# Kernel optimization log

Hardware: AMD Instinct MI355X
Metric: run time of the kernel (lower is better)

The kernel has to match this reference:

```python
import jax, jax.numpy as jnp
import numpy as np

B, C, H, W = 4, 64, 64, 64
C8 = C // 8
TEMPERATURE = 1.0


def setup_inputs() -> dict:
    key = jax.random.key(0)
    ks = jax.random.split(key, 8)
    x = jax.random.normal(ks[0], (B, C, H, W), jnp.float32)
    s = 1.0 / np.sqrt(C).astype(np.float32)
    wq = jax.random.normal(ks[1], (C8, C), jnp.float32) * s
    bq = jax.random.normal(ks[2], (C8,), jnp.float32) * 0.01
    wk = jax.random.normal(ks[3], (C8, C), jnp.float32) * s
    bk = jax.random.normal(ks[4], (C8,), jnp.float32) * 0.01
    wv = jax.random.normal(ks[5], (C, C), jnp.float32) * s
    bv = jax.random.normal(ks[6], (C,), jnp.float32) * 0.01
    fractal_weight = jnp.asarray(0.5, jnp.float32)
    noise = jax.random.normal(ks[7], (B, H * W, H * W), jnp.float32)
    return {"x": x, "wq": wq, "bq": bq, "wk": wk, "bk": bk,
            "wv": wv, "bv": bv, "fractal_weight": fractal_weight, "noise": noise}


def _conv1x1(x, w, b):
    # 1x1 conv == per-pixel matmul: [B,C,H,W] x [O,C] -> [B,O,H,W]
    return jnp.einsum('bchw,oc->bohw', x, w) + b[None, :, None, None]


def _fractal_reg(amap):
    # amap: [B,1,H,W]; unbiased variance of avg-pooled maps at scales 1,2,4,8
    b, _, h, w = amap.shape
    variances = []
    for s in (1, 2, 4, 8):
        p = amap.reshape(b, 1, h // s, s, w // s, s).mean(axis=(3, 5))  # avg_pool2d
        m = p.mean(axis=(2, 3), keepdims=True)
        n = (h // s) * (w // s)
        variances.append(((p - m) ** 2).sum(axis=(2, 3)) / (n - 1))  # [B,1]
    top = jnp.stack(variances[:-1])
    bot = jnp.stack(variances[1:])
    return (top / bot).mean()


def reference(x, wq, bq, wk, bk, wv, bv, fractal_weight, noise):
    b, c, h, w = x.shape
    n = h * w
    q = _conv1x1(x, wq, bq).reshape(b, -1, n).transpose(0, 2, 1)  # [B,N,C8]
    k = _conv1x1(x, wk, bk).reshape(b, -1, n)                     # [B,C8,N]
    v = _conv1x1(x, wv, bv).reshape(b, -1, n)                     # [B,C,N]
    attn = jax.nn.softmax(jnp.einsum('bnc,bcm->bnm', q, k) * TEMPERATURE, axis=-1)
    chaos = noise * 0.1 * fractal_weight
    attn = jax.nn.softmax(attn + chaos, axis=-1)                  # [B,N,N]
    # out[b,c,i] = sum_j v[b,c,j] * attn[i,j]  (bmm(value, attn^T))
    out = jnp.einsum('bcj,bij->bci', v, attn).reshape(b, c, h, w)
    amap = attn.mean(axis=-1).reshape(b, 1, h, w)
    reg = _fractal_reg(amap)
    return out, reg
```

## Files before the change

kernel.cpp:

```cpp
#include <hip/hip_runtime.h>
#include <hip/hip_bf16.h>
#include <math.h>

#define LOG2E 1.4426950408889634f

typedef __attribute__((ext_vector_type(8))) short short8_t;
typedef __attribute__((ext_vector_type(4))) float float4_t;

union Frag { short8_t f; unsigned u[4]; };

__device__ inline unsigned pack_bf16(float lo, float hi){
  union { __hip_bfloat162 h2; unsigned u; } cv;
  cv.h2 = __float22bfloat162_rn(make_float2(lo, hi));
  return cv.u;
}

__global__ __launch_bounds__(256) void k1_qkv(
    const float* __restrict__ x, const float* __restrict__ wq, const float* __restrict__ bq,
    const float* __restrict__ wk, const float* __restrict__ bk,
    const float* __restrict__ wv, const float* __restrict__ bv,
    float* __restrict__ qs, float* __restrict__ kk, unsigned short* __restrict__ vT,
    float* __restrict__ regout)
{
  int tid = blockIdx.x*256 + threadIdx.x;
  if (tid == 0) regout[0] = 0.f;
  int g = tid >> 14;
  int p = tid & 16383;
  int b = p >> 12, n = p & 4095;
  const float* xp = x + (size_t)b*64*4096 + n;
  float xr[64];
  #pragma unroll
  for (int c=0;c<64;++c) xr[c] = xp[(size_t)c*4096];

  if (g == 0){
    float* qp = qs + ((size_t)b*4096 + n)*8;
    #pragma unroll
    for (int u=0;u<8;++u){
      const float* wr = wq + u*64;
      float a0=0,a1=0,a2=0,a3=0;
      #pragma unroll
      for (int c=0;c<64;c+=4){ a0=fmaf(wr[c],xr[c],a0); a1=fmaf(wr[c+1],xr[c+1],a1);
                               a2=fmaf(wr[c+2],xr[c+2],a2); a3=fmaf(wr[c+3],xr[c+3],a3); }
      qp[u] = (bq[u] + ((a0+a1)+(a2+a3))) * LOG2E;
    }
    #pragma unroll
    for (int u=0;u<8;++u){
      const float* wr = wk + u*64;
      float a0=0,a1=0,a2=0,a3=0;
      #pragma unroll
      for (int c=0;c<64;c+=4){ a0=fmaf(wr[c],xr[c],a0); a1=fmaf(wr[c+1],xr[c+1],a1);
                               a2=fmaf(wr[c+2],xr[c+2],a2); a3=fmaf(wr[c+3],xr[c+3],a3); }
      kk[((size_t)b*8+u)*4096 + n] = bk[u] + ((a0+a1)+(a2+a3));
    }
  } else {
    int c0 = (g==1) ? 0 : (g==2) ? 22 : 43;
    int c1 = (g==1) ? 22 : (g==2) ? 43 : 64;
    for (int u=c0; u<c1; ++u){
      const float* wr = wv + u*64;
      float a0=0,a1=0,a2=0,a3=0;
      #pragma unroll
      for (int c=0;c<64;c+=4){ a0=fmaf(wr[c],xr[c],a0); a1=fmaf(wr[c+1],xr[c+1],a1);
                               a2=fmaf(wr[c+2],xr[c+2],a2); a3=fmaf(wr[c+3],xr[c+3],a3); }
      float res = bv[u] + ((a0+a1)+(a2+a3));
      __hip_bfloat16 h = __float2bfloat16(res);
      vT[((size_t)b*64+u)*4096 + n] = *(unsigned short*)&h;
    }
  }
}

__global__ __launch_bounds__(512, 8) void k3_fused(
    const float* __restrict__ qs, const float* __restrict__ kk,
    const unsigned short* __restrict__ vT, const float* __restrict__ noise,
    const float* __restrict__ fwp, float* __restrict__ out)
{
  __shared__ float lds_l[8][16];
  __shared__ float lds_acc[8][16][64];
  int bid = blockIdx.x;
  int b = bid >> 8; int i0 = (bid & 255) * 16;
  int t = threadIdx.x; int w = t >> 6; int lane = t & 63;
  int li = lane & 15, q4 = lane >> 4;
  int row = i0 + li;
  int jbase = w * 512;

  const float* qp = qs + ((size_t)b*4096 + row)*8;
  float qv[8];
  #pragma unroll
  for (int c=0;c<8;++c) qv[c] = qp[c];
  const float* kkb = kk + (size_t)b*8*4096;
  const float* nzr = noise + ((size_t)b*4096 + row)*4096;
  const unsigned short* vTb = vT + (size_t)b*64*4096;

  float l1 = 0.f;
  for (int sc=0; sc<16; ++sc){
    int j0 = jbase + sc*32 + q4*8;
    float s0=0,s1=0,s2=0,s3=0,s4=0,s5=0,s6=0,s7=0;
    #pragma unroll
    for (int c=0;c<8;++c){
      const float4* kp = (const float4*)(kkb + (size_t)c*4096 + j0);
      float4 ka = kp[0], kb2 = kp[1];
      float q = qv[c];
      s0=fmaf(q,ka.x,s0); s1=fmaf(q,ka.y,s1); s2=fmaf(q,ka.z,s2); s3=fmaf(q,ka.w,s3);
      s4=fmaf(q,kb2.x,s4); s5=fmaf(q,kb2.y,s5); s6=fmaf(q,kb2.z,s6); s7=fmaf(q,kb2.w,s7);
    }
    l1 += exp2f(s0-25.f); l1 += exp2f(s1-25.f); l1 += exp2f(s2-25.f); l1 += exp2f(s3-25.f);
    l1 += exp2f(s4-25.f); l1 += exp2f(s5-25.f); l1 += exp2f(s6-25.f); l1 += exp2f(s7-25.f);
  }
  l1 += __shfl_xor(l1, 16); l1 += __shfl_xor(l1, 32);
  if (lane < 16) lds_l[w][li] = l1;
  __syncthreads();
  float l1tot = 0.f;
  #pragma unroll
  for (int ww=0; ww<8; ++ww) l1tot += lds_l[ww][li];
  float c1 = LOG2E / l1tot;
  float ncoef = 0.1f * fwp[0] * LOG2E;

  float4_t acc0 = {0.f,0.f,0.f,0.f}, acc1 = acc0, acc2 = acc0, acc3 = acc0;
  float l2 = 0.f;
  for (int sc=0; sc<16; ++sc){
    int j0 = jbase + sc*32 + q4*8;
    float s0=0,s1=0,s2=0,s3=0,s4=0,s5=0,s6=0,s7=0;
    #pragma unroll
    for (int c=0;c<8;++c){
      const float4* kp = (const float4*)(kkb + (size_t)c*4096 + j0);
      float4 ka = kp[0], kb2 = kp[1];
      float q = qv[c];
      s0=fmaf(q,ka.x,s0); s1=fmaf(q,ka.y,s1); s2=fmaf(q,ka.z,s2); s3=fmaf(q,ka.w,s3);
      s4=fmaf(q,kb2.x,s4); s5=fmaf(q,kb2.y,s5); s6=fmaf(q,kb2.z,s6); s7=fmaf(q,kb2.w,s7);
    }
    const float4* np = (const float4*)(nzr + j0);
    float4 n0 = np[0], n1 = np[1];
    float p0,p1,p2,p3,p4,p5,p6,p7;
    p0 = exp2f(fmaf(ncoef,n0.x, fmaf(exp2f(s0-25.f), c1, -2.f)));
    p1 = exp2f(fmaf(ncoef,n0.y, fmaf(exp2f(s1-25.f), c1, -2.f)));
    p2 = exp2f(fmaf(ncoef,n0.z, fmaf(exp2f(s2-25.f), c1, -2.f)));
    p3 = exp2f(fmaf(ncoef,n0.w, fmaf(exp2f(s3-25.f), c1, -2.f)));
    p4 = exp2f(fmaf(ncoef,n1.x, fmaf(exp2f(s4-25.f), c1, -2.f)));
    p5 = exp2f(fmaf(ncoef,n1.y, fmaf(exp2f(s5-25.f), c1, -2.f)));
    p6 = exp2f(fmaf(ncoef,n1.z, fmaf(exp2f(s6-25.f), c1, -2.f)));
    p7 = exp2f(fmaf(ncoef,n1.w, fmaf(exp2f(s7-25.f), c1, -2.f)));
    l2 += ((p0+p1)+(p2+p3)) + ((p4+p5)+(p6+p7));
    Frag af;
    af.u[0] = pack_bf16(p0,p1); af.u[1] = pack_bf16(p2,p3);
    af.u[2] = pack_bf16(p4,p5); af.u[3] = pack_bf16(p6,p7);
    const unsigned short* vp = vTb + (size_t)li*4096 + j0;
    short8_t b0 = *(const short8_t*)(vp);
    short8_t b1 = *(const short8_t*)(vp + 16*4096);
    short8_t b2 = *(const short8_t*)(vp + 32*4096);
    short8_t b3 = *(const short8_t*)(vp + 48*4096);
    acc0 = __builtin_amdgcn_mfma_f32_16x16x32_bf16(af.f, b0, acc0, 0, 0, 0);
    acc1 = __builtin_amdgcn_mfma_f32_16x16x32_bf16(af.f, b1, acc1, 0, 0, 0);
    acc2 = __builtin_amdgcn_mfma_f32_16x16x32_bf16(af.f, b2, acc2, 0, 0, 0);
    acc3 = __builtin_amdgcn_mfma_f32_16x16x32_bf16(af.f, b3, acc3, 0, 0, 0);
  }
  l2 += __shfl_xor(l2, 16); l2 += __shfl_xor(l2, 32);
  __syncthreads();
  if (lane < 16) lds_l[w][li] = l2;
  #pragma unroll
  for (int reg=0; reg<4; ++reg){
    int rr = q4*4 + reg;
    lds_acc[w][rr][ 0 + li] = acc0[reg];
    lds_acc[w][rr][16 + li] = acc1[reg];
    lds_acc[w][rr][32 + li] = acc2[reg];
    lds_acc[w][rr][48 + li] = acc3[reg];
  }
  __syncthreads();
  if (t < 256){
    int c = t >> 2, rg = t & 3;
    float4 o;
    float* op = (float*)&o;
    #pragma unroll
    for (int r=0;r<4;++r){
      int rr = rg*4 + r;
      float vsum = 0.f, l2t = 0.f;
      #pragma unroll
      for (int ww=0; ww<8; ++ww){ vsum += lds_acc[ww][rr][c]; l2t += lds_l[ww][rr]; }
      op[r] = vsum / l2t;
    }
    *(float4*)(out + ((size_t)b*64 + c)*4096 + i0 + rg*4) = o;
  }
}

extern "C" void kernel_launch(void* const* d_in, const int* in_sizes, int n_in,
                              void* d_out, int out_size, void* d_ws, size_t ws_size,
                              hipStream_t stream) {
  const float* x     = (const float*)d_in[0];
  const float* wq    = (const float*)d_in[1];
  const float* bq    = (const float*)d_in[2];
  const float* wk    = (const float*)d_in[3];
  const float* bk    = (const float*)d_in[4];
  const float* wv    = (const float*)d_in[5];
  const float* bv    = (const float*)d_in[6];
  const float* fw    = (const float*)d_in[7];
  const float* noise = (const float*)d_in[8];
  float* out = (float*)d_out;
  float* ws  = (float*)d_ws;
  float* qs = ws;
  float* kk = ws + 131072;
  unsigned short* vT = (unsigned short*)(ws + 262144);

  hipLaunchKernelGGL(k1_qkv,   dim3(256),  dim3(256), 0, stream,
                     x,wq,bq,wk,bk,wv,bv,qs,kk,vT, out + 1048576);
  hipLaunchKernelGGL(k3_fused, dim3(1024), dim3(512), 0, stream,
                     qs,kk,vT,noise,fw,out);
}
```

Baseline: 547.6 us.

## Spread QKV projection over more blocks and schedule loads ahead in attention loop

The projection kernel now runs 16 thread groups instead of 4 (q and k each split in two, v split twelve ways), so it launches 1024 blocks for more parallelism, at the cost of re-reading x per group. In the fused attention kernel, the noise and V loads are moved ahead of the score and exp math, and sched_group_barrier hints group VMEM loads and VALU and MFMA work to hide memory latency. Launch bounds drop from 8 to 4 waves per EU, which allows more registers but may reduce occupancy.

New measurement: 540.8 us. About the same (-1.2%).

```diff
diff --git a/kernel.cpp b/kernel.cpp
--- a/kernel.cpp
+++ b/kernel.cpp
@@ -32,10 +32,12 @@
   #pragma unroll
   for (int c=0;c<64;++c) xr[c] = xp[(size_t)c*4096];
 
-  if (g == 0){
+  if (g < 2){
     float* qp = qs + ((size_t)b*4096 + n)*8;
+    int u0 = g*4;
     #pragma unroll
-    for (int u=0;u<8;++u){
+    for (int uu=0;uu<4;++uu){
+      int u = u0 + uu;
       const float* wr = wq + u*64;
       float a0=0,a1=0,a2=0,a3=0;
       #pragma unroll
@@ -43,8 +45,11 @@
                                a2=fmaf(wr[c+2],xr[c+2],a2); a3=fmaf(wr[c+3],xr[c+3],a3); }
       qp[u] = (bq[u] + ((a0+a1)+(a2+a3))) * LOG2E;
     }
+  } else if (g < 4){
+    int u0 = (g-2)*4;
     #pragma unroll
-    for (int u=0;u<8;++u){
+    for (int uu=0;uu<4;++uu){
+      int u = u0 + uu;
       const float* wr = wk + u*64;
       float a0=0,a1=0,a2=0,a3=0;
       #pragma unroll
@@ -53,9 +58,9 @@
       kk[((size_t)b*8+u)*4096 + n] = bk[u] + ((a0+a1)+(a2+a3));
     }
   } else {
-    int c0 = (g==1) ? 0 : (g==2) ? 22 : 43;
-    int c1 = (g==1) ? 22 : (g==2) ? 43 : 64;
-    for (int u=c0; u<c1; ++u){
+    int c0 = ((g-4)*64)/12;
+    int c1v = ((g-3)*64)/12;
+    for (int u=c0; u<c1v; ++u){
       const float* wr = wv + u*64;
       float a0=0,a1=0,a2=0,a3=0;
       #pragma unroll
@@ -68,7 +73,19 @@
   }
 }
 
-__global__ __launch_bounds__(512, 8) void k3_fused(
+
+#define PB_DOT(J0) \
+    float s0=0,s1=0,s2=0,s3=0,s4=0,s5=0,s6=0,s7=0; \
+    _Pragma("unroll") \
+    for (int c=0;c<8;++c){ \
+      const float4* kp = (const float4*)(kkb + (size_t)c*4096 + (J0)); \
+      float4 ka = kp[0], kb2 = kp[1]; \
+      float q = qv[c]; \
+      s0=fmaf(q,ka.x,s0); s1=fmaf(q,ka.y,s1); s2=fmaf(q,ka.z,s2); s3=fmaf(q,ka.w,s3); \
+      s4=fmaf(q,kb2.x,s4); s5=fmaf(q,kb2.y,s5); s6=fmaf(q,kb2.z,s6); s7=fmaf(q,kb2.w,s7); \
+    }
+
+__global__ __launch_bounds__(512, 4) void k3_fused(
     const float* __restrict__ qs, const float* __restrict__ kk,
     const unsigned short* __restrict__ vT, const float* __restrict__ noise,
     const float* __restrict__ fwp, float* __restrict__ out)
@@ -93,17 +110,11 @@
   float l1 = 0.f;
   for (int sc=0; sc<16; ++sc){
     int j0 = jbase + sc*32 + q4*8;
-    float s0=0,s1=0,s2=0,s3=0,s4=0,s5=0,s6=0,s7=0;
-    #pragma unroll
-    for (int c=0;c<8;++c){
-      const float4* kp = (const float4*)(kkb + (size_t)c*4096 + j0);
-      float4 ka = kp[0], kb2 = kp[1];
-      float q = qv[c];
-      s0=fmaf(q,ka.x,s0); s1=fmaf(q,ka.y,s1); s2=fmaf(q,ka.z,s2); s3=fmaf(q,ka.w,s3);
-      s4=fmaf(q,kb2.x,s4); s5=fmaf(q,kb2.y,s5); s6=fmaf(q,kb2.z,s6); s7=fmaf(q,kb2.w,s7);
-    }
+    PB_DOT(j0)
     l1 += exp2f(s0-25.f); l1 += exp2f(s1-25.f); l1 += exp2f(s2-25.f); l1 += exp2f(s3-25.f);
     l1 += exp2f(s4-25.f); l1 += exp2f(s5-25.f); l1 += exp2f(s6-25.f); l1 += exp2f(s7-25.f);
+    __builtin_amdgcn_sched_group_barrier(0x20, 16, 0);
+    __builtin_amdgcn_sched_group_barrier(0x02, 76, 0);
   }
   l1 += __shfl_xor(l1, 16); l1 += __shfl_xor(l1, 32);
   if (lane < 16) lds_l[w][li] = l1;
@@ -116,19 +127,18 @@
 
   float4_t acc0 = {0.f,0.f,0.f,0.f}, acc1 = acc0, acc2 = acc0, acc3 = acc0;
   float l2 = 0.f;
+  const unsigned short* vbase = vTb + (size_t)li*4096;
+
   for (int sc=0; sc<16; ++sc){
     int j0 = jbase + sc*32 + q4*8;
-    float s0=0,s1=0,s2=0,s3=0,s4=0,s5=0,s6=0,s7=0;
-    #pragma unroll
-    for (int c=0;c<8;++c){
-      const float4* kp = (const float4*)(kkb + (size_t)c*4096 + j0);
-      float4 ka = kp[0], kb2 = kp[1];
-      float q = qv[c];
-      s0=fmaf(q,ka.x,s0); s1=fmaf(q,ka.y,s1); s2=fmaf(q,ka.z,s2); s3=fmaf(q,ka.w,s3);
-      s4=fmaf(q,kb2.x,s4); s5=fmaf(q,kb2.y,s5); s6=fmaf(q,kb2.z,s6); s7=fmaf(q,kb2.w,s7);
-    }
     const float4* np = (const float4*)(nzr + j0);
     float4 n0 = np[0], n1 = np[1];
+    PB_DOT(j0)
+    const unsigned short* vp = vbase + j0;
+    short8_t b0 = *(const short8_t*)(vp);
+    short8_t b1 = *(const short8_t*)(vp + 16*4096);
+    short8_t b2 = *(const short8_t*)(vp + 32*4096);
+    short8_t b3 = *(const short8_t*)(vp + 48*4096);
     float p0,p1,p2,p3,p4,p5,p6,p7;
     p0 = exp2f(fmaf(ncoef,n0.x, fmaf(exp2f(s0-25.f), c1, -2.f)));
     p1 = exp2f(fmaf(ncoef,n0.y, fmaf(exp2f(s1-25.f), c1, -2.f)));
@@ -142,16 +152,17 @@
     Frag af;
     af.u[0] = pack_bf16(p0,p1); af.u[1] = pack_bf16(p2,p3);
     af.u[2] = pack_bf16(p4,p5); af.u[3] = pack_bf16(p6,p7);
-    const unsigned short* vp = vTb + (size_t)li*4096 + j0;
-    short8_t b0 = *(const short8_t*)(vp);
-    short8_t b1 = *(const short8_t*)(vp + 16*4096);
-    short8_t b2 = *(const short8_t*)(vp + 32*4096);
-    short8_t b3 = *(const short8_t*)(vp + 48*4096);
     acc0 = __builtin_amdgcn_mfma_f32_16x16x32_bf16(af.f, b0, acc0, 0, 0, 0);
     acc1 = __builtin_amdgcn_mfma_f32_16x16x32_bf16(af.f, b1, acc1, 0, 0, 0);
     acc2 = __builtin_amdgcn_mfma_f32_16x16x32_bf16(af.f, b2, acc2, 0, 0, 0);
     acc3 = __builtin_amdgcn_mfma_f32_16x16x32_bf16(af.f, b3, acc3, 0, 0, 0);
-  }
+    __builtin_amdgcn_sched_group_barrier(0x20, 18, 0);
+    __builtin_amdgcn_sched_group_barrier(0x02, 60, 0);
+    __builtin_amdgcn_sched_group_barrier(0x20,  4, 0);
+    __builtin_amdgcn_sched_group_barrier(0x02, 48, 0);
+    __builtin_amdgcn_sched_group_barrier(0x08,  4, 0);
+  }
+
   l2 += __shfl_xor(l2, 16); l2 += __shfl_xor(l2, 32);
   __syncthreads();
   if (lane < 16) lds_l[w][li] = l2;
@@ -198,7 +209,7 @@
   float* kk = ws + 131072;
   unsigned short* vT = (unsigned short*)(ws + 262144);
 
-  hipLaunchKernelGGL(k1_qkv,   dim3(256),  dim3(256), 0, stream,
+  hipLaunchKernelGGL(k1_qkv,   dim3(1024), dim3(256), 0, stream,
                      x,wq,bq,wk,bk,wv,bv,qs,kk,vT, out + 1048576);
   hipLaunchKernelGGL(k3_fused, dim3(1024), dim3(512), 0, stream,
                      qs,kk,vT,noise,fw,out);
```
